# Performance work log

Measured on AMD Instinct MI355X. Metric: run time of the kernel, lower is better.

The kernel has to match this reference:

```python
import jax, jax.numpy as jnp
import numpy as np
import math

B = 8
H_GRID, W_GRID = 24, 24          # patch grid (24x24 -> 576 patches)
P = H_GRID * W_GRID              # 576
TOP_N = 3                        # TOKEN_CONFIGS[192]['top_n_per_region']
NUM_TOKENS = 336                 # Stage1_CONFIGS[192]
K = min(math.ceil(NUM_TOKENS / B), 144 * TOP_N)
DIST_THRESH = math.sqrt(280.0)   # distance=280
HEADS = 16
D = 1024
N_LAYERS_SIM = 9                 # hidden_states[16:25]


def _dist_penalty():
    # penalty(i,j) = max(0, 1 - dist2d(i,j)/threshold), shape [P, P]
    ys, xs = jnp.meshgrid(jnp.arange(H_GRID), jnp.arange(W_GRID), indexing='ij')
    coords = jnp.stack([ys, xs], axis=-1).reshape(-1, 2).astype(jnp.float32)
    diff = coords[:, None, :] - coords[None, :, :]
    dist = jnp.sqrt(jnp.sum(diff * diff, axis=-1))
    return 1.0 - jnp.minimum(dist / DIST_THRESH, 1.0)


def setup_inputs() -> dict:
    key = jax.random.key(0)
    k1, k2, k3 = jax.random.split(key, 3)
    attn = jax.random.uniform(k1, (B, HEADS, P + 1, P + 1), dtype=jnp.float32)
    hidden_agg = jax.random.normal(k2, (B, P + 1, D), dtype=jnp.float32)
    stacked_hs = jax.random.normal(k3, (N_LAYERS_SIM, B, P + 1, D), dtype=jnp.float32)
    return {"attn": attn, "hidden_agg": hidden_agg, "stacked_hs": stacked_hs}


def reference(attn, hidden_agg, stacked_hs):
    dist_penalty = _dist_penalty()                      # [P, P]

    # CLS-attention importance metric
    cls_attn = attn[:, :, 0, 1:]                        # [B, heads, P]
    metric = cls_attn.sum(axis=1)                       # [B, P]

    # region-wise (2x2 blocks) top-n selection
    m2d = metric.reshape(B, H_GRID // 2, 2, W_GRID // 2, 2)
    regions = m2d.transpose(0, 1, 3, 2, 4).reshape(B, -1, 4)   # [B, 144, 4]
    _, loc = jax.lax.top_k(regions, TOP_N)              # [B, 144, TOP_N]
    ly, lx = loc // 2, loc % 2
    rid = jnp.arange(144)
    ry, rx = rid // (W_GRID // 2), rid % (W_GRID // 2)
    gy = ry[None, :, None] * 2 + ly
    gx = rx[None, :, None] * 2 + lx
    cand = (gy * W_GRID + gx).reshape(B, -1)            # [B, 144*TOP_N]

    # global top-K over regional candidates
    cand_scores = jnp.take_along_axis(metric, cand, axis=1)
    _, top_c = jax.lax.top_k(cand_scores, K)
    bench = jnp.take_along_axis(cand, top_c, axis=1)
    bench = jnp.sort(bench, axis=1)                     # [B, K]

    # cosine similarity of layer-averaged patch tokens
    avg_hs = stacked_hs.mean(axis=0)[:, 1:, :]          # [B, P, D]
    nrm = avg_hs / jnp.maximum(jnp.linalg.norm(avg_hs, axis=-1, keepdims=True), 1e-12)
    bench_nrm = jnp.take_along_axis(nrm, bench[..., None], axis=1)  # [B, K, D]
    sim_rows = jnp.einsum('bkd,bpd->bkp', bench_nrm, nrm)           # [B, K, P]

    w = jax.nn.relu(sim_rows) * dist_penalty[bench]     # [B, K, P]
    w = w / (w.sum(axis=-1, keepdims=True) + 1e-8)
    # self weight = 1.0 (scatter_)
    b_idx = jnp.arange(B)[:, None]
    k_idx = jnp.arange(K)[None, :]
    w = w.at[b_idx, k_idx, bench].set(1.0)

    patch_agg = hidden_agg[:, 1:, :]                    # [B, P, D]
    out = jnp.einsum('bkp,bpd->bkd', w, patch_agg)      # [B, K, D]
    return out, bench
```

## Files before the change

kernel.cpp:

```cpp
#include <hip/hip_runtime.h>
#include <stdint.h>

#define B_ 8
#define HGRID 24
#define PN 576
#define PP1 577
#define HEADS 16
#define DD 1024
#define NL 9
#define KS 42
#define NREG 144
#define NCAND 432
#define KSPLIT 4
#define DIST_THRESH_F 16.733200530681511f

__device__ __forceinline__ float dist_penalty(int q, int p) {
    float dy = (float)(q / HGRID) - (float)(p / HGRID);
    float dx = (float)(q % HGRID) - (float)(p % HGRID);
    float d = sqrtf(dy * dy + dx * dx);
    return 1.0f - fminf(d / DIST_THRESH_F, 1.0f);
}

__global__ __launch_bounds__(512) void select_kernel(const float* __restrict__ attn,
                                                     int* __restrict__ bench_out,
                                                     float* __restrict__ bench_f_out) {
    __shared__ float ms[PN];
    __shared__ int cand[NCAND];
    __shared__ float csc[NCAND];
    __shared__ int sel[KS];
    int b = blockIdx.x;
    int tid = threadIdx.x;
    const size_t plane = (size_t)PP1 * PP1;
    for (int p = tid; p < PN; p += 512) {
        size_t base = (size_t)b * HEADS * plane + 1 + p;
        float s = 0.f;
#pragma unroll
        for (int h = 0; h < HEADS; ++h) s += attn[base + (size_t)h * plane];
        ms[p] = s;
    }
    __syncthreads();
    if (tid < NREG) {
        int ry = tid / 12, rx = tid % 12;
        float v[4]; int pid[4];
#pragma unroll
        for (int e = 0; e < 4; ++e) {
            int gy = ry * 2 + (e >> 1), gx = rx * 2 + (e & 1);
            pid[e] = gy * HGRID + gx;
            v[e] = ms[pid[e]];
        }
        bool used[4] = {false, false, false, false};
#pragma unroll
        for (int n = 0; n < 3; ++n) {
            int best = -1; float bv = -1e30f;
#pragma unroll
            for (int e = 0; e < 4; ++e)
                if (!used[e] && v[e] > bv) { bv = v[e]; best = e; }
            used[best] = true;
            cand[tid * 3 + n] = pid[best];
        }
    }
    __syncthreads();
    if (tid < NCAND) csc[tid] = ms[cand[tid]];
    __syncthreads();
    if (tid < NCAND) {
        float myv = csc[tid];
        int rank = 0;
#pragma unroll 8
        for (int j = 0; j < NCAND; ++j) {
            float vj = csc[j];
            rank += (int)((vj > myv) || (vj == myv && j < tid));
        }
        if (rank < KS) sel[rank] = cand[tid];
    }
    __syncthreads();
    if (tid < KS) {
        int v = sel[tid];
        int r2 = 0;
#pragma unroll
        for (int j = 0; j < KS; ++j) r2 += (int)(sel[j] < v);
        bench_out[b * KS + r2] = v;
        bench_f_out[b * KS + r2] = (float)v;
    }
}

__global__ __launch_bounds__(256) void nrm_kernel(const float* __restrict__ shs,
                                                  float* __restrict__ nrm) {
    int blk = blockIdx.x;
    int b = blk / PN, p = blk % PN;
    int t = threadIdx.x;
    const size_t lstride = (size_t)B_ * PP1 * DD;
    size_t rowbase = ((size_t)b * PP1 + (p + 1)) * DD + t * 4;
    float4 acc = make_float4(0.f, 0.f, 0.f, 0.f);
#pragma unroll
    for (int l = 0; l < NL; ++l) {
        const float4 v = *reinterpret_cast<const float4*>(shs + rowbase + (size_t)l * lstride);
        acc.x += v.x; acc.y += v.y; acc.z += v.z; acc.w += v.w;
    }
    acc.x /= 9.0f; acc.y /= 9.0f; acc.z /= 9.0f; acc.w /= 9.0f;
    float ss = acc.x * acc.x + acc.y * acc.y + acc.z * acc.z + acc.w * acc.w;
#pragma unroll
    for (int o = 32; o > 0; o >>= 1) ss += __shfl_down(ss, o, 64);
    __shared__ float wsum[4];
    int lane = t & 63, wv = t >> 6;
    if (lane == 0) wsum[wv] = ss;
    __syncthreads();
    float total = wsum[0] + wsum[1] + wsum[2] + wsum[3];
    float scale = 1.0f / fmaxf(sqrtf(total), 1e-12f);
    float4 o4 = make_float4(acc.x * scale, acc.y * scale, acc.z * scale, acc.w * scale);
    *reinterpret_cast<float4*>(nrm + ((size_t)b * PN + p) * DD + t * 4) = o4;
}

__global__ __launch_bounds__(256) void sim_kernel(const float* __restrict__ nrm,
                                                  const int* __restrict__ bench,
                                                  float* __restrict__ wpart) {
    __shared__ __align__(16) float As[48][68];
    __shared__ __align__(16) float Bs[32][68];
    __shared__ int bsh[KS];
    int tile = blockIdx.x;
    int b = blockIdx.y;
    int kc = blockIdx.z;
    int tid = threadIdx.x;
    int tm = tid >> 4, tn = tid & 15;
    int p0 = tile * 32;
    if (tid < KS) bsh[tid] = bench[b * KS + tid];
    for (int i = tid; i < 6 * 68; i += 256) As[42 + i / 68][i % 68] = 0.f;
    float acc[3][2] = {};
    const float* nb = nrm + (size_t)b * PN * DD;
    for (int c = kc * 4; c < kc * 4 + 4; ++c) {
        int d0 = c * 64;
        __syncthreads();
#pragma unroll
        for (int it = 0; it < 3; ++it) {
            int idx = it * 256 + tid;
            if (idx < 672) {
                int row = idx >> 4, col = (idx & 15) * 4;
                float4 v = *reinterpret_cast<const float4*>(nb + (size_t)bsh[row] * DD + d0 + col);
                *reinterpret_cast<float4*>(&As[row][col]) = v;
            }
        }
#pragma unroll
        for (int it = 0; it < 2; ++it) {
            int idx = it * 256 + tid;
            int row = idx >> 4, col = (idx & 15) * 4;
            float4 v = *reinterpret_cast<const float4*>(nb + (size_t)(p0 + row) * DD + d0 + col);
            *reinterpret_cast<float4*>(&Bs[row][col]) = v;
        }
        __syncthreads();
#pragma unroll
        for (int kk = 0; kk < 64; kk += 4) {
            float4 a0 = *reinterpret_cast<const float4*>(&As[tm * 3 + 0][kk]);
            float4 a1 = *reinterpret_cast<const float4*>(&As[tm * 3 + 1][kk]);
            float4 a2 = *reinterpret_cast<const float4*>(&As[tm * 3 + 2][kk]);
            float4 b0 = *reinterpret_cast<const float4*>(&Bs[tn * 2 + 0][kk]);
            float4 b1 = *reinterpret_cast<const float4*>(&Bs[tn * 2 + 1][kk]);
            acc[0][0] += a0.x * b0.x + a0.y * b0.y + a0.z * b0.z + a0.w * b0.w;
            acc[0][1] += a0.x * b1.x + a0.y * b1.y + a0.z * b1.z + a0.w * b1.w;
            acc[1][0] += a1.x * b0.x + a1.y * b0.y + a1.z * b0.z + a1.w * b0.w;
            acc[1][1] += a1.x * b1.x + a1.y * b1.y + a1.z * b1.z + a1.w * b1.w;
            acc[2][0] += a2.x * b0.x + a2.y * b0.y + a2.z * b0.z + a2.w * b0.w;
            acc[2][1] += a2.x * b1.x + a2.y * b1.y + a2.z * b1.z + a2.w * b1.w;
        }
    }
    float* wp = wpart + (size_t)kc * B_ * KS * PN;
#pragma unroll
    for (int i = 0; i < 3; ++i) {
        int k = tm * 3 + i;
        if (k >= KS) continue;
#pragma unroll
        for (int j = 0; j < 2; ++j) {
            int p = p0 + tn * 2 + j;
            wp[((size_t)b * KS + k) * PN + p] = acc[i][j];
        }
    }
}

__global__ __launch_bounds__(256) void wnorm_kernel(const float* __restrict__ wpart,
                                                    float* __restrict__ w,
                                                    const int* __restrict__ bench) {
    int blk = blockIdx.x;
    int q = bench[blk];
    const size_t kcs = (size_t)B_ * KS * PN;
    const float* row0 = wpart + (size_t)blk * PN;
    int t = threadIdx.x;
    float v[3];
    int pidx[3] = {t, t + 256, t + 512};
#pragma unroll
    for (int u = 0; u < 3; ++u) {
        int p = pidx[u];
        if (u < 2 || t < 64) {
            float s = row0[p] + row0[p + kcs] + row0[p + 2 * kcs] + row0[p + 3 * kcs];
            v[u] = fmaxf(s, 0.f) * dist_penalty(q, p);
        } else v[u] = 0.f;
    }
    float s = v[0] + v[1] + v[2];
#pragma unroll
    for (int o = 32; o > 0; o >>= 1) s += __shfl_down(s, o, 64);
    __shared__ float ws4[4];
    int lane = t & 63, wv = t >> 6;
    if (lane == 0) ws4[wv] = s;
    __syncthreads();
    float total = ws4[0] + ws4[1] + ws4[2] + ws4[3];
    float scale = 1.0f / (total + 1e-8f);
    float* orow = w + (size_t)blk * PN;
    orow[t] = (t == q) ? 1.0f : v[0] * scale;
    orow[t + 256] = (t + 256 == q) ? 1.0f : v[1] * scale;
    if (t < 64) orow[t + 512] = (t + 512 == q) ? 1.0f : v[2] * scale;
}

__global__ __launch_bounds__(256) void out_kernel(const float* __restrict__ w,
                                                  const float* __restrict__ hidden,
                                                  float* __restrict__ out) {
    __shared__ __align__(16) float As[48][36];
    __shared__ __align__(16) float Bs[32][36];
    int ntile = blockIdx.x;
    int b = blockIdx.y;
    int tid = threadIdx.x;
    int tm = tid >> 4, tn = tid & 15;
    int n0 = ntile * 32;
    for (int i = tid; i < 6 * 36; i += 256) As[42 + i / 36][i % 36] = 0.f;
    float acc[3][2] = {};
    const float* wb = w + (size_t)b * KS * PN;
    const float* hb = hidden + ((size_t)b * PP1 + 1) * DD;
    for (int c = 0; c < 18; ++c) {
        int p0 = c * 32;
        __syncthreads();
#pragma unroll
        for (int it = 0; it < 2; ++it) {
            int idx = it * 256 + tid;
            if (idx < 336) {
                int row = idx >> 3, col = (idx & 7) * 4;
                float4 v = *reinterpret_cast<const float4*>(wb + (size_t)row * PN + p0 + col);
                *reinterpret_cast<float4*>(&As[row][col]) = v;
            }
        }
        {
            int row = tid >> 3, col = (tid & 7) * 4;
            float4 v = *reinterpret_cast<const float4*>(hb + (size_t)(p0 + row) * DD + n0 + col);
            *reinterpret_cast<float4*>(&Bs[row][col]) = v;
        }
        __syncthreads();
#pragma unroll
        for (int kk = 0; kk < 32; ++kk) {
            float a0 = As[tm * 3 + 0][kk], a1 = As[tm * 3 + 1][kk], a2 = As[tm * 3 + 2][kk];
            float b0 = Bs[kk][tn * 2 + 0], b1 = Bs[kk][tn * 2 + 1];
            acc[0][0] += a0 * b0; acc[0][1] += a0 * b1;
            acc[1][0] += a1 * b0; acc[1][1] += a1 * b1;
            acc[2][0] += a2 * b0; acc[2][1] += a2 * b1;
        }
    }
#pragma unroll
    for (int i = 0; i < 3; ++i) {
        int k = tm * 3 + i;
        if (k >= KS) continue;
#pragma unroll
        for (int j = 0; j < 2; ++j)
            out[((size_t)b * KS + k) * DD + n0 + tn * 2 + j] = acc[i][j];
    }
}

extern "C" void kernel_launch(void* const* d_in, const int* in_sizes, int n_in,
                              void* d_out, int out_size, void* d_ws, size_t ws_size,
                              hipStream_t stream) {
    const float* attn = (const float*)d_in[0];
    const float* hidden = (const float*)d_in[1];
    const float* shs = (const float*)d_in[2];
    float* out = (float*)d_out;
    float* bench_f = out + (size_t)B_ * KS * DD;

    char* ws = (char*)d_ws;
    float* nrm = (float*)ws;
    int* bench = (int*)(ws + 18874368);
    float* wpart = (float*)(ws + 18874368 + 1536);
    float* w = (float*)(ws + 18874368 + 1536 + 3096576);

    select_kernel<<<dim3(B_), dim3(512), 0, stream>>>(attn, bench, bench_f);
    nrm_kernel<<<dim3(B_ * PN), dim3(256), 0, stream>>>(shs, nrm);
    sim_kernel<<<dim3(18, B_, KSPLIT), dim3(256), 0, stream>>>(nrm, bench, wpart);
    wnorm_kernel<<<dim3(B_ * KS), dim3(256), 0, stream>>>(wpart, w, bench);
    out_kernel<<<dim3(32, B_), dim3(256), 0, stream>>>(w, hidden, out);
}
```

Measured before the change: 378.0 us.

## Fuse select into nrm kernel, double sim K-split, vectorise out_kernel LDS reads

```diff
diff --git a/kernel.cpp b/kernel.cpp
--- a/kernel.cpp
+++ b/kernel.cpp
@@ -11,7 +11,8 @@
 #define KS 42
 #define NREG 144
 #define NCAND 432
-#define KSPLIT 4
+#define KSPLIT 8
+#define NRM_BLOCKS 2304
 #define DIST_THRESH_F 16.733200530681511f
 
 __device__ __forceinline__ float dist_penalty(int q, int p) {
@@ -21,93 +22,98 @@
     return 1.0f - fminf(d / DIST_THRESH_F, 1.0f);
 }
 
-__global__ __launch_bounds__(512) void select_kernel(const float* __restrict__ attn,
-                                                     int* __restrict__ bench_out,
-                                                     float* __restrict__ bench_f_out) {
-    __shared__ float ms[PN];
-    __shared__ int cand[NCAND];
-    __shared__ float csc[NCAND];
-    __shared__ int sel[KS];
-    int b = blockIdx.x;
+__global__ __launch_bounds__(512) void nrm_select_kernel(const float* __restrict__ shs,
+                                                         const float* __restrict__ attn,
+                                                         float* __restrict__ nrm,
+                                                         int* __restrict__ bench_out,
+                                                         float* __restrict__ bench_f_out) {
+    int blk = blockIdx.x;
     int tid = threadIdx.x;
-    const size_t plane = (size_t)PP1 * PP1;
-    for (int p = tid; p < PN; p += 512) {
-        size_t base = (size_t)b * HEADS * plane + 1 + p;
-        float s = 0.f;
-#pragma unroll
-        for (int h = 0; h < HEADS; ++h) s += attn[base + (size_t)h * plane];
-        ms[p] = s;
-    }
-    __syncthreads();
-    if (tid < NREG) {
-        int ry = tid / 12, rx = tid % 12;
-        float v[4]; int pid[4];
-#pragma unroll
-        for (int e = 0; e < 4; ++e) {
-            int gy = ry * 2 + (e >> 1), gx = rx * 2 + (e & 1);
-            pid[e] = gy * HGRID + gx;
-            v[e] = ms[pid[e]];
-        }
-        bool used[4] = {false, false, false, false};
-#pragma unroll
-        for (int n = 0; n < 3; ++n) {
-            int best = -1; float bv = -1e30f;
-#pragma unroll
-            for (int e = 0; e < 4; ++e)
-                if (!used[e] && v[e] > bv) { bv = v[e]; best = e; }
-            used[best] = true;
-            cand[tid * 3 + n] = pid[best];
-        }
-    }
-    __syncthreads();
-    if (tid < NCAND) csc[tid] = ms[cand[tid]];
-    __syncthreads();
-    if (tid < NCAND) {
-        float myv = csc[tid];
-        int rank = 0;
+    if (blk < NRM_BLOCKS) {
+        __shared__ float wsum[8];
+        int half = tid >> 8;
+        int th = tid & 255;
+        int r = blk * 2 + half;
+        int b = r / PN, p = r % PN;
+        const size_t lstride = (size_t)B_ * PP1 * DD;
+        size_t rowbase = ((size_t)b * PP1 + (p + 1)) * DD + th * 4;
+        float4 acc = make_float4(0.f, 0.f, 0.f, 0.f);
+#pragma unroll
+        for (int l = 0; l < NL; ++l) {
+            const float4 v = *reinterpret_cast<const float4*>(shs + rowbase + (size_t)l * lstride);
+            acc.x += v.x; acc.y += v.y; acc.z += v.z; acc.w += v.w;
+        }
+        acc.x /= 9.0f; acc.y /= 9.0f; acc.z /= 9.0f; acc.w /= 9.0f;
+        float ss = acc.x * acc.x + acc.y * acc.y + acc.z * acc.z + acc.w * acc.w;
+#pragma unroll
+        for (int o = 32; o > 0; o >>= 1) ss += __shfl_down(ss, o, 64);
+        int lane = tid & 63, wv = tid >> 6;
+        if (lane == 0) wsum[wv] = ss;
+        __syncthreads();
+        float total = wsum[half * 4 + 0] + wsum[half * 4 + 1] + wsum[half * 4 + 2] + wsum[half * 4 + 3];
+        float scale = 1.0f / fmaxf(sqrtf(total), 1e-12f);
+        float4 o4 = make_float4(acc.x * scale, acc.y * scale, acc.z * scale, acc.w * scale);
+        *reinterpret_cast<float4*>(nrm + (size_t)r * DD + th * 4) = o4;
+        return;
+    }
+    {
+        __shared__ float ms[PN];
+        __shared__ int cand[NCAND];
+        __shared__ float csc[NCAND];
+        __shared__ int sel[KS];
+        int b = blk - NRM_BLOCKS;
+        const size_t plane = (size_t)PP1 * PP1;
+        for (int p = tid; p < PN; p += 512) {
+            size_t base = (size_t)b * HEADS * plane + 1 + p;
+            float s = 0.f;
+#pragma unroll
+            for (int h = 0; h < HEADS; ++h) s += attn[base + (size_t)h * plane];
+            ms[p] = s;
+        }
+        __syncthreads();
+        if (tid < NREG) {
+            int ry = tid / 12, rx = tid % 12;
+            float v[4]; int pid[4];
+#pragma unroll
+            for (int e = 0; e < 4; ++e) {
+                int gy = ry * 2 + (e >> 1), gx = rx * 2 + (e & 1);
+                pid[e] = gy * HGRID + gx;
+                v[e] = ms[pid[e]];
+            }
+            bool used[4] = {false, false, false, false};
+#pragma unroll
+            for (int n = 0; n < 3; ++n) {
+                int best = -1; float bv = -1e30f;
+#pragma unroll
+                for (int e = 0; e < 4; ++e)
+                    if (!used[e] && v[e] > bv) { bv = v[e]; best = e; }
+                used[best] = true;
+                cand[tid * 3 + n] = pid[best];
+            }
+        }
+        __syncthreads();
+        if (tid < NCAND) csc[tid] = ms[cand[tid]];
+        __syncthreads();
+        if (tid < NCAND) {
+            float myv = csc[tid];
+            int rank = 0;
 #pragma unroll 8
-        for (int j = 0; j < NCAND; ++j) {
-            float vj = csc[j];
-            rank += (int)((vj > myv) || (vj == myv && j < tid));
-        }
-        if (rank < KS) sel[rank] = cand[tid];
-    }
-    __syncthreads();
-    if (tid < KS) {
-        int v = sel[tid];
-        int r2 = 0;
-#pragma unroll
-        for (int j = 0; j < KS; ++j) r2 += (int)(sel[j] < v);
-        bench_out[b * KS + r2] = v;
-        bench_f_out[b * KS + r2] = (float)v;
-    }
-}
-
-__global__ __launch_bounds__(256) void nrm_kernel(const float* __restrict__ shs,
-                                                  float* __restrict__ nrm) {
-    int blk = blockIdx.x;
-    int b = blk / PN, p = blk % PN;
-    int t = threadIdx.x;
-    const size_t lstride = (size_t)B_ * PP1 * DD;
-    size_t rowbase = ((size_t)b * PP1 + (p + 1)) * DD + t * 4;
-    float4 acc = make_float4(0.f, 0.f, 0.f, 0.f);
-#pragma unroll
-    for (int l = 0; l < NL; ++l) {
-        const float4 v = *reinterpret_cast<const float4*>(shs + rowbase + (size_t)l * lstride);
-        acc.x += v.x; acc.y += v.y; acc.z += v.z; acc.w += v.w;
-    }
-    acc.x /= 9.0f; acc.y /= 9.0f; acc.z /= 9.0f; acc.w /= 9.0f;
-    float ss = acc.x * acc.x + acc.y * acc.y + acc.z * acc.z + acc.w * acc.w;
-#pragma unroll
-    for (int o = 32; o > 0; o >>= 1) ss += __shfl_down(ss, o, 64);
-    __shared__ float wsum[4];
-    int lane = t & 63, wv = t >> 6;
-    if (lane == 0) wsum[wv] = ss;
-    __syncthreads();
-    float total = wsum[0] + wsum[1] + wsum[2] + wsum[3];
-    float scale = 1.0f / fmaxf(sqrtf(total), 1e-12f);
-    float4 o4 = make_float4(acc.x * scale, acc.y * scale, acc.z * scale, acc.w * scale);
-    *reinterpret_cast<float4*>(nrm + ((size_t)b * PN + p) * DD + t * 4) = o4;
+            for (int j = 0; j < NCAND; ++j) {
+                float vj = csc[j];
+                rank += (int)((vj > myv) || (vj == myv && j < tid));
+            }
+            if (rank < KS) sel[rank] = cand[tid];
+        }
+        __syncthreads();
+        if (tid < KS) {
+            int v = sel[tid];
+            int r2 = 0;
+#pragma unroll
+            for (int j = 0; j < KS; ++j) r2 += (int)(sel[j] < v);
+            bench_out[b * KS + r2] = v;
+            bench_f_out[b * KS + r2] = (float)v;
+        }
+    }
 }
 
 __global__ __launch_bounds__(256) void sim_kernel(const float* __restrict__ nrm,
@@ -126,7 +132,7 @@
     for (int i = tid; i < 6 * 68; i += 256) As[42 + i / 68][i % 68] = 0.f;
     float acc[3][2] = {};
     const float* nb = nrm + (size_t)b * PN * DD;
-    for (int c = kc * 4; c < kc * 4 + 4; ++c) {
+    for (int c = kc * 2; c < kc * 2 + 2; ++c) {
         int d0 = c * 64;
         __syncthreads();
 #pragma unroll
@@ -188,7 +194,9 @@
     for (int u = 0; u < 3; ++u) {
         int p = pidx[u];
         if (u < 2 || t < 64) {
-            float s = row0[p] + row0[p + kcs] + row0[p + 2 * kcs] + row0[p + 3 * kcs];
+            float s = 0.f;
+#pragma unroll
+            for (int i = 0; i < KSPLIT; ++i) s += row0[p + (size_t)i * kcs];
             v[u] = fmaxf(s, 0.f) * dist_penalty(q, p);
         } else v[u] = 0.f;
     }
@@ -240,12 +248,20 @@
         }
         __syncthreads();
 #pragma unroll
-        for (int kk = 0; kk < 32; ++kk) {
-            float a0 = As[tm * 3 + 0][kk], a1 = As[tm * 3 + 1][kk], a2 = As[tm * 3 + 2][kk];
-            float b0 = Bs[kk][tn * 2 + 0], b1 = Bs[kk][tn * 2 + 1];
-            acc[0][0] += a0 * b0; acc[0][1] += a0 * b1;
-            acc[1][0] += a1 * b0; acc[1][1] += a1 * b1;
-            acc[2][0] += a2 * b0; acc[2][1] += a2 * b1;
+        for (int kk = 0; kk < 32; kk += 4) {
+            float4 a0 = *reinterpret_cast<const float4*>(&As[tm * 3 + 0][kk]);
+            float4 a1 = *reinterpret_cast<const float4*>(&As[tm * 3 + 1][kk]);
+            float4 a2 = *reinterpret_cast<const float4*>(&As[tm * 3 + 2][kk]);
+            const float* a0f = reinterpret_cast<const float*>(&a0);
+            const float* a1f = reinterpret_cast<const float*>(&a1);
+            const float* a2f = reinterpret_cast<const float*>(&a2);
+#pragma unroll
+            for (int j = 0; j < 4; ++j) {
+                float2 bv = *reinterpret_cast<const float2*>(&Bs[kk + j][tn * 2]);
+                acc[0][0] += a0f[j] * bv.x; acc[0][1] += a0f[j] * bv.y;
+                acc[1][0] += a1f[j] * bv.x; acc[1][1] += a1f[j] * bv.y;
+                acc[2][0] += a2f[j] * bv.x; acc[2][1] += a2f[j] * bv.y;
+            }
         }
     }
 #pragma unroll
@@ -271,10 +287,9 @@
     float* nrm = (float*)ws;
     int* bench = (int*)(ws + 18874368);
     float* wpart = (float*)(ws + 18874368 + 1536);
-    float* w = (float*)(ws + 18874368 + 1536 + 3096576);
-
-    select_kernel<<<dim3(B_), dim3(512), 0, stream>>>(attn, bench, bench_f);
-    nrm_kernel<<<dim3(B_ * PN), dim3(256), 0, stream>>>(shs, nrm);
+    float* w = (float*)(ws + 18874368 + 1536 + 6193152);
+
+    nrm_select_kernel<<<dim3(NRM_BLOCKS + B_), dim3(512), 0, stream>>>(shs, attn, nrm, bench, bench_f);
     sim_kernel<<<dim3(18, B_, KSPLIT), dim3(256), 0, stream>>>(nrm, bench, wpart);
     wnorm_kernel<<<dim3(B_ * KS), dim3(256), 0, stream>>>(wpart, w, bench);
     out_kernel<<<dim3(32, B_), dim3(256), 0, stream>>>(w, hidden, out);
```

New measurement: 378.7 us. About the same (+0.2%).
